# Kernel optimization log

Hardware: AMD Instinct MI355X
Metric: run time of the kernel (lower is better)

Reference implementation:

```python
import jax, jax.numpy as jnp
import numpy as np

N_BOOKS = 8
TAU_Q = 5.0

def setup_inputs() -> dict:
    key = jax.random.key(0)
    k1, k2, k3 = jax.random.split(key, 3)
    N, D_in = 65536, 512
    D = 512          # N_books * L_word
    N_words = 256
    x = jax.random.normal(k1, (N, D_in), dtype=jnp.float32)
    # xavier-uniform-like scale for fc weight [D_out, D_in]
    lim_w = float(np.sqrt(6.0 / (D_in + D)))
    W = jax.random.uniform(k2, (D, D_in), dtype=jnp.float32, minval=-lim_w, maxval=lim_w)
    b = jnp.zeros((D,), dtype=jnp.float32)
    lim_c = float(np.sqrt(6.0 / (N_words + D)))
    C = jax.random.uniform(k3, (N_words, D), dtype=jnp.float32, minval=-lim_c, maxval=lim_c)
    return {"x": x, "W": W, "b": b, "C": C}

def reference(x, W, b, C):
    # fc: X = x @ W^T + b  -> [N, D]
    X = x @ W.T + b
    N, D = X.shape
    M = C.shape[0]
    L = D // N_BOOKS
    Xb = X.reshape(N, N_BOOKS, L)          # [N, B, L]
    Cb = C.reshape(M, N_BOOKS, L)          # [M, B, L]
    x2 = jnp.sum(Xb * Xb, axis=-1)[:, :, None]           # [N, B, 1]
    c2 = jnp.sum(Cb * Cb, axis=-1).T[None, :, :]         # [1, B, M]
    xc = jnp.einsum('nbl,mbl->nbm', Xb, Cb)              # [N, B, M]
    dist = x2 + c2 - 2.0 * xc
    soft = jax.nn.softmax(-TAU_Q * dist, axis=-1)        # softmax over codewords
    # weighted codebook sum per book, then concat books -> [N, D]
    Z = jnp.einsum('nbm,mbl->nbl', soft, Cb).reshape(N, D)
    return X, Z
```

## Files before the change

kernel.cpp:

```cpp
#include <hip/hip_runtime.h>
#include <cstdint>
#include <cstddef>

#define N_ROWS   65536
#define D_IN     512
#define D_OUT    512
#define N_WORDS  256
#define N_BOOKS  8
#define TAU      5.0f
#define LOG2E    1.44269504088896340736f

typedef __attribute__((ext_vector_type(8))) short short8;
typedef __attribute__((ext_vector_type(4))) float f32x4;

__device__ __forceinline__ unsigned short f2bf(float f) {
    __bf16 h = (__bf16)f;
    return __builtin_bit_cast(unsigned short, h);
}
__device__ __forceinline__ float bf2f(unsigned short h) {
    unsigned u = ((unsigned)h) << 16;
    return __builtin_bit_cast(float, u);
}

__global__ __launch_bounds__(256) void prep_codebook(
        const float* __restrict__ C, const float* __restrict__ W,
        unsigned short* __restrict__ packA, unsigned short* __restrict__ packB,
        unsigned short* __restrict__ packW, float* __restrict__ nc2) {
    const int gid = blockIdx.x * 256 + threadIdx.x;
    if (gid < 131072) {
        const int i  = gid & 7;
        const int l  = (gid >> 3) & 63;
        const int mf = (gid >> 9) & 15;
        const int ks = (gid >> 13) & 1;
        const int b  = gid >> 14;
        const int row = (l & 15) + 16 * mf;
        const int col = b * 64 + (l >> 4) * 8 + i + 32 * ks;
        packA[gid] = f2bf(C[(size_t)row * D_IN + col]);
    } else if (gid < 262144) {
        const int g   = gid - 131072;
        const int i   = g & 7;
        const int l   = (g >> 3) & 63;
        const int n2  = (g >> 9) & 3;
        const int ks2 = (g >> 11) & 7;
        const int b   = g >> 14;
        const int m   = 32 * ks2 + 16 * (i >> 2) + 4 * (l >> 4) + (i & 3);
        const int col = b * 64 + n2 * 16 + (l & 15);
        packB[g] = f2bf(C[(size_t)m * D_IN + col]);
    } else if (gid < 524288) {
        const int h  = gid - 262144;
        const int i  = h & 7;
        const int l  = (h >> 3) & 63;
        const int cf = (h >> 9) & 7;
        const int kk = (h >> 12) & 15;
        const int bn = h >> 16;
        packW[h] = f2bf(W[(size_t)(bn * 128 + cf * 16 + (l & 15)) * D_IN
                          + kk * 32 + (l >> 4) * 8 + i]);
    } else if (gid < 526336) {
        const int t = gid - 524288;
        const int b = t >> 8, m = t & 255;
        const float* cp = C + (size_t)m * D_IN + b * 64;
        float s = 0.f;
        for (int l = 0; l < 64; ++l) {
            const float v = bf2f(f2bf(cp[l]));
            s = fmaf(v, v, s);
        }
        nc2[t] = -TAU * LOG2E * s;
    }
}

__global__ __launch_bounds__(512, 1) void fused_fc_quant(
        const float* __restrict__ x, const unsigned short* __restrict__ packW,
        const float* __restrict__ bias,
        const unsigned short* __restrict__ packA,
        const unsigned short* __restrict__ packB,
        const float* __restrict__ nc2g,
        float* __restrict__ X, float* __restrict__ Z) {
    __shared__ unsigned short Asm[2][64 * 40];
    __shared__ __attribute__((aligned(16))) unsigned short Xb[8][32 * 72];
    __shared__ float nc2s[2048];

    const int tid  = threadIdx.x;
    const int n0   = blockIdx.x * 64;
    const int lane = tid & 63;
    const int w    = tid >> 6;
    const int lo = lane & 15, hi = lane >> 4;
    const int bn  = w >> 1;
    const int wc4 = (w & 1) * 4;

    const int row_s = tid >> 3;
    const int fq    = (tid & 7) << 2;

    reinterpret_cast<float4*>(nc2s)[tid] = reinterpret_cast<const float4*>(nc2g)[tid];

    float biasv[4];
    #pragma unroll
    for (int cf = 0; cf < 4; ++cf) biasv[cf] = bias[w * 64 + cf * 16 + lo];

    f32x4 acc[4][4];
    #pragma unroll
    for (int i = 0; i < 4; ++i)
        #pragma unroll
        for (int j = 0; j < 4; ++j) acc[i][j] = (f32x4){0.f, 0.f, 0.f, 0.f};

    float4 rx[2];
    short8 rw[2][4];
    rx[0] = *reinterpret_cast<const float4*>(&x[(size_t)(n0 + row_s) * D_IN + fq]);
    #pragma unroll
    for (int cf = 0; cf < 4; ++cf)
        rw[0][cf] = *reinterpret_cast<const short8*>(
            packW + ((size_t)((bn * 16 + 0) * 8 + wc4 + cf) * 64 + lane) * 8);
    {
        ushort4 p;
        p.x = f2bf(rx[0].x); p.y = f2bf(rx[0].y);
        p.z = f2bf(rx[0].z); p.w = f2bf(rx[0].w);
        *reinterpret_cast<ushort4*>(&Asm[0][row_s * 40 + fq]) = p;
    }
    rx[1] = *reinterpret_cast<const float4*>(&x[(size_t)(n0 + row_s) * D_IN + 32 + fq]);
    #pragma unroll
    for (int cf = 0; cf < 4; ++cf)
        rw[1][cf] = *reinterpret_cast<const short8*>(
            packW + ((size_t)((bn * 16 + 1) * 8 + wc4 + cf) * 64 + lane) * 8);
    __syncthreads();

    #pragma unroll
    for (int kk = 0; kk < 16; ++kk) {
        const int cur = kk & 1;
        short8 aW[4];
        #pragma unroll
        for (int cf = 0; cf < 4; ++cf) aW[cf] = rw[cur][cf];
        if (kk < 14) {
            rx[cur] = *reinterpret_cast<const float4*>(
                &x[(size_t)(n0 + row_s) * D_IN + (kk + 2) * 32 + fq]);
            #pragma unroll
            for (int cf = 0; cf < 4; ++cf)
                rw[cur][cf] = *reinterpret_cast<const short8*>(
                    packW + ((size_t)((bn * 16 + kk + 2) * 8 + wc4 + cf) * 64 + lane) * 8);
        }
        short8 a[4];
        #pragma unroll
        for (int fm = 0; fm < 4; ++fm)
            a[fm] = *reinterpret_cast<const short8*>(&Asm[cur][(fm * 16 + lo) * 40 + hi * 8]);
        #pragma unroll
        for (int fm = 0; fm < 4; ++fm)
            #pragma unroll
            for (int cf = 0; cf < 4; ++cf)
                acc[fm][cf] = __builtin_amdgcn_mfma_f32_16x16x32_bf16(
                    a[fm], aW[cf], acc[fm][cf], 0, 0, 0);
        if (kk < 15) {
            const float4 v = rx[cur ^ 1];
            ushort4 p;
            p.x = f2bf(v.x); p.y = f2bf(v.y); p.z = f2bf(v.z); p.w = f2bf(v.w);
            *reinterpret_cast<ushort4*>(&Asm[cur ^ 1][row_s * 40 + fq]) = p;
            __syncthreads();
        }
    }

    const float S2 = 2.0f * TAU * LOG2E;
    #pragma unroll
    for (int h = 0; h < 2; ++h) {
        #pragma unroll
        for (int fmh = 0; fmh < 2; ++fmh) {
            const int fm = h * 2 + fmh;
            #pragma unroll
            for (int cf = 0; cf < 4; ++cf)
                #pragma unroll
                for (int j = 0; j < 4; ++j) {
                    const float v = acc[fm][cf][j] + biasv[cf];
                    __builtin_nontemporal_store(
                        v, &X[(size_t)(n0 + h * 32 + fmh * 16 + hi * 4 + j) * D_OUT
                              + w * 64 + cf * 16 + lo]);
                    Xb[w][(fmh * 16 + hi * 4 + j) * 72 + cf * 16 + lo] = f2bf(v);
                }
        }
        asm volatile("s_waitcnt lgkmcnt(0)" ::: "memory");

        short8 xf[2][2];
        #pragma unroll
        for (int g = 0; g < 2; ++g)
            #pragma unroll
            for (int ks = 0; ks < 2; ++ks)
                xf[g][ks] = *reinterpret_cast<const short8*>(
                    &Xb[w][(g * 16 + lo) * 72 + ks * 32 + hi * 8]);

        f32x4 qa[2][16];
        #pragma unroll
        for (int g = 0; g < 2; ++g)
            #pragma unroll
            for (int mf = 0; mf < 16; ++mf) qa[g][mf] = (f32x4){0.f, 0.f, 0.f, 0.f};
        #pragma unroll
        for (int ks = 0; ks < 2; ++ks)
            #pragma unroll
            for (int mf = 0; mf < 16; ++mf) {
                const short8 cfr = *reinterpret_cast<const short8*>(
                    packA + ((size_t)((w * 2 + ks) * 16 + mf) * 64 + lane) * 8);
                qa[0][mf] = __builtin_amdgcn_mfma_f32_16x16x32_bf16(cfr, xf[0][ks], qa[0][mf], 0, 0, 0);
                qa[1][mf] = __builtin_amdgcn_mfma_f32_16x16x32_bf16(cfr, xf[1][ks], qa[1][mf], 0, 0, 0);
            }

        float inv[2];
        #pragma unroll
        for (int g = 0; g < 2; ++g) {
            float s = 0.f;
            #pragma unroll
            for (int mf = 0; mf < 16; ++mf) {
                const f32x4 nv = *reinterpret_cast<const f32x4*>(
                    &nc2s[w * 256 + mf * 16 + hi * 4]);
                const float p0 = exp2f(fmaf(qa[g][mf][0], S2, nv[0]));
                const float p1 = exp2f(fmaf(qa[g][mf][1], S2, nv[1]));
                const float p2 = exp2f(fmaf(qa[g][mf][2], S2, nv[2]));
                const float p3 = exp2f(fmaf(qa[g][mf][3], S2, nv[3]));
                qa[g][mf][0] = p0; qa[g][mf][1] = p1;
                qa[g][mf][2] = p2; qa[g][mf][3] = p3;
                s += (p0 + p1) + (p2 + p3);
            }
            s += __shfl_xor(s, 16, 64);
            s += __shfl_xor(s, 32, 64);
            inv[g] = 1.0f / s;
        }

        f32x4 acc2[2][4];
        #pragma unroll
        for (int g = 0; g < 2; ++g)
            #pragma unroll
            for (int n2 = 0; n2 < 4; ++n2) acc2[g][n2] = (f32x4){0.f, 0.f, 0.f, 0.f};
        #pragma unroll
        for (int ks2 = 0; ks2 < 8; ++ks2) {
            short8 pa[2];
            #pragma unroll
            for (int g = 0; g < 2; ++g) {
                pa[g][0] = (short)f2bf(qa[g][2 * ks2][0]);
                pa[g][1] = (short)f2bf(qa[g][2 * ks2][1]);
                pa[g][2] = (short)f2bf(qa[g][2 * ks2][2]);
                pa[g][3] = (short)f2bf(qa[g][2 * ks2][3]);
                pa[g][4] = (short)f2bf(qa[g][2 * ks2 + 1][0]);
                pa[g][5] = (short)f2bf(qa[g][2 * ks2 + 1][1]);
                pa[g][6] = (short)f2bf(qa[g][2 * ks2 + 1][2]);
                pa[g][7] = (short)f2bf(qa[g][2 * ks2 + 1][3]);
            }
            #pragma unroll
            for (int n2 = 0; n2 < 4; ++n2) {
                const short8 bv = *reinterpret_cast<const short8*>(
                    packB + ((size_t)((w * 8 + ks2) * 4 + n2) * 64 + lane) * 8);
                acc2[0][n2] = __builtin_amdgcn_mfma_f32_16x16x32_bf16(pa[0], bv, acc2[0][n2], 0, 0, 0);
                acc2[1][n2] = __builtin_amdgcn_mfma_f32_16x16x32_bf16(pa[1], bv, acc2[1][n2], 0, 0, 0);
            }
        }

        #pragma unroll
        for (int g = 0; g < 2; ++g) {
            float invr[4];
            #pragma unroll
            for (int j = 0; j < 4; ++j) invr[j] = __shfl(inv[g], hi * 4 + j, 64);
            #pragma unroll
            for (int n2 = 0; n2 < 4; ++n2)
                #pragma unroll
                for (int j = 0; j < 4; ++j)
                    __builtin_nontemporal_store(
                        acc2[g][n2][j] * invr[j],
                        &Z[(size_t)(n0 + h * 32 + g * 16 + hi * 4 + j) * D_OUT
                           + w * 64 + n2 * 16 + lo]);
        }
    }
}

extern "C" void kernel_launch(void* const* d_in, const int* in_sizes, int n_in,
                              void* d_out, int out_size, void* d_ws, size_t ws_size,
                              hipStream_t stream) {
    const float* x = (const float*)d_in[0];
    const float* W = (const float*)d_in[1];
    const float* b = (const float*)d_in[2];
    const float* C = (const float*)d_in[3];

    float* X = (float*)d_out;
    float* Z = X + (size_t)N_ROWS * D_OUT;

    unsigned short* packA = (unsigned short*)d_ws;
    unsigned short* packB = packA + 131072;
    unsigned short* packW = packB + 131072;
    float*          nc2g  = (float*)(packW + 262144);

    prep_codebook<<<dim3(2056), dim3(256), 0, stream>>>(C, W, packA, packB, packW, nc2g);
    fused_fc_quant<<<dim3(N_ROWS / 64), dim3(512), 0, stream>>>(
        x, packW, b, packA, packB, nc2g, X, Z);
}
```

Measured before the change: 168.2 us.

## Halve rows per block, stage full x tile in LDS, pack softmax probs early

Each block now handles 32 rows instead of 64. The whole 32x512 x tile is converted to bf16 and staged in LDS up front, which removes the per-k-step double buffering and the barriers inside the FC loop. The quantization stage processes the codeword dimension in two halves and packs the exp values straight into bf16 pairs, so fewer live fp32 registers are needed. The launch bound no longer forces one block per CU, aiming for higher occupancy. The cost is twice as many blocks, so packW, packA and packB are re-read twice as often per row, and the LDS footprint per block grows.

```diff
diff --git a/kernel.cpp b/kernel.cpp
--- a/kernel.cpp
+++ b/kernel.cpp
@@ -12,6 +12,7 @@
 
 typedef __attribute__((ext_vector_type(8))) short short8;
 typedef __attribute__((ext_vector_type(4))) float f32x4;
+typedef __attribute__((ext_vector_type(4))) unsigned uint4v;
 
 __device__ __forceinline__ unsigned short f2bf(float f) {
     __bf16 h = (__bf16)f;
@@ -68,198 +69,190 @@
     }
 }
 
-__global__ __launch_bounds__(512, 1) void fused_fc_quant(
+__global__ __launch_bounds__(512) void fused_fc_quant(
         const float* __restrict__ x, const unsigned short* __restrict__ packW,
         const float* __restrict__ bias,
         const unsigned short* __restrict__ packA,
         const unsigned short* __restrict__ packB,
         const float* __restrict__ nc2g,
         float* __restrict__ X, float* __restrict__ Z) {
-    __shared__ unsigned short Asm[2][64 * 40];
+    __shared__ __attribute__((aligned(16))) unsigned short xAll[32 * 520];
     __shared__ __attribute__((aligned(16))) unsigned short Xb[8][32 * 72];
     __shared__ float nc2s[2048];
 
     const int tid  = threadIdx.x;
-    const int n0   = blockIdx.x * 64;
+    const int n0   = blockIdx.x * 32;
     const int lane = tid & 63;
     const int w    = tid >> 6;
     const int lo = lane & 15, hi = lane >> 4;
     const int bn  = w >> 1;
     const int wc4 = (w & 1) * 4;
 
-    const int row_s = tid >> 3;
-    const int fq    = (tid & 7) << 2;
-
     reinterpret_cast<float4*>(nc2s)[tid] = reinterpret_cast<const float4*>(nc2g)[tid];
 
+    #pragma unroll
+    for (int it = 0; it < 8; ++it) {
+        const int idx = it * 512 + tid;
+        const int row = idx >> 7;
+        const int f4  = idx & 127;
+        const float4 v = *reinterpret_cast<const float4*>(
+            &x[(size_t)(n0 + row) * D_IN + f4 * 4]);
+        ushort4 p;
+        p.x = f2bf(v.x); p.y = f2bf(v.y); p.z = f2bf(v.z); p.w = f2bf(v.w);
+        *reinterpret_cast<ushort4*>(&xAll[row * 520 + f4 * 4]) = p;
+    }
+
     float biasv[4];
     #pragma unroll
     for (int cf = 0; cf < 4; ++cf) biasv[cf] = bias[w * 64 + cf * 16 + lo];
 
-    f32x4 acc[4][4];
-    #pragma unroll
-    for (int i = 0; i < 4; ++i)
-        #pragma unroll
-        for (int j = 0; j < 4; ++j) acc[i][j] = (f32x4){0.f, 0.f, 0.f, 0.f};
-
-    float4 rx[2];
+    __syncthreads();
+
+    f32x4 acc[2][4];
+    #pragma unroll
+    for (int fm = 0; fm < 2; ++fm)
+        #pragma unroll
+        for (int cf = 0; cf < 4; ++cf) acc[fm][cf] = (f32x4){0.f, 0.f, 0.f, 0.f};
+
     short8 rw[2][4];
-    rx[0] = *reinterpret_cast<const float4*>(&x[(size_t)(n0 + row_s) * D_IN + fq]);
-    #pragma unroll
-    for (int cf = 0; cf < 4; ++cf)
+    #pragma unroll
+    for (int cf = 0; cf < 4; ++cf) {
         rw[0][cf] = *reinterpret_cast<const short8*>(
             packW + ((size_t)((bn * 16 + 0) * 8 + wc4 + cf) * 64 + lane) * 8);
-    {
-        ushort4 p;
-        p.x = f2bf(rx[0].x); p.y = f2bf(rx[0].y);
-        p.z = f2bf(rx[0].z); p.w = f2bf(rx[0].w);
-        *reinterpret_cast<ushort4*>(&Asm[0][row_s * 40 + fq]) = p;
-    }
-    rx[1] = *reinterpret_cast<const float4*>(&x[(size_t)(n0 + row_s) * D_IN + 32 + fq]);
-    #pragma unroll
-    for (int cf = 0; cf < 4; ++cf)
         rw[1][cf] = *reinterpret_cast<const short8*>(
             packW + ((size_t)((bn * 16 + 1) * 8 + wc4 + cf) * 64 + lane) * 8);
-    __syncthreads();
-
+    }
     #pragma unroll
     for (int kk = 0; kk < 16; ++kk) {
-        const int cur = kk & 1;
         short8 aW[4];
         #pragma unroll
-        for (int cf = 0; cf < 4; ++cf) aW[cf] = rw[cur][cf];
+        for (int cf = 0; cf < 4; ++cf) aW[cf] = rw[kk & 1][cf];
         if (kk < 14) {
-            rx[cur] = *reinterpret_cast<const float4*>(
-                &x[(size_t)(n0 + row_s) * D_IN + (kk + 2) * 32 + fq]);
             #pragma unroll
             for (int cf = 0; cf < 4; ++cf)
-                rw[cur][cf] = *reinterpret_cast<const short8*>(
+                rw[kk & 1][cf] = *reinterpret_cast<const short8*>(
                     packW + ((size_t)((bn * 16 + kk + 2) * 8 + wc4 + cf) * 64 + lane) * 8);
         }
-        short8 a[4];
-        #pragma unroll
-        for (int fm = 0; fm < 4; ++fm)
-            a[fm] = *reinterpret_cast<const short8*>(&Asm[cur][(fm * 16 + lo) * 40 + hi * 8]);
-        #pragma unroll
-        for (int fm = 0; fm < 4; ++fm)
+        short8 a[2];
+        #pragma unroll
+        for (int fm = 0; fm < 2; ++fm)
+            a[fm] = *reinterpret_cast<const short8*>(
+                &xAll[(fm * 16 + lo) * 520 + kk * 32 + hi * 8]);
+        #pragma unroll
+        for (int fm = 0; fm < 2; ++fm)
             #pragma unroll
             for (int cf = 0; cf < 4; ++cf)
                 acc[fm][cf] = __builtin_amdgcn_mfma_f32_16x16x32_bf16(
                     a[fm], aW[cf], acc[fm][cf], 0, 0, 0);
-        if (kk < 15) {
-            const float4 v = rx[cur ^ 1];
-            ushort4 p;
-            p.x = f2bf(v.x); p.y = f2bf(v.y); p.z = f2bf(v.z); p.w = f2bf(v.w);
-            *reinterpret_cast<ushort4*>(&Asm[cur ^ 1][row_s * 40 + fq]) = p;
-            __syncthreads();
-        }
-    }
+    }
+
+    #pragma unroll
+    for (int fm = 0; fm < 2; ++fm)
+        #pragma unroll
+        for (int cf = 0; cf < 4; ++cf)
+            #pragma unroll
+            for (int j = 0; j < 4; ++j) {
+                const float v = acc[fm][cf][j] + biasv[cf];
+                __builtin_nontemporal_store(
+                    v, &X[(size_t)(n0 + fm * 16 + hi * 4 + j) * D_OUT
+                          + w * 64 + cf * 16 + lo]);
+                Xb[w][(fm * 16 + hi * 4 + j) * 72 + cf * 16 + lo] = f2bf(v);
+            }
+    asm volatile("s_waitcnt lgkmcnt(0)" ::: "memory");
+
+    short8 xf[2][2];
+    #pragma unroll
+    for (int g = 0; g < 2; ++g)
+        #pragma unroll
+        for (int ks = 0; ks < 2; ++ks)
+            xf[g][ks] = *reinterpret_cast<const short8*>(
+                &Xb[w][(g * 16 + lo) * 72 + ks * 32 + hi * 8]);
 
     const float S2 = 2.0f * TAU * LOG2E;
-    #pragma unroll
-    for (int h = 0; h < 2; ++h) {
-        #pragma unroll
-        for (int fmh = 0; fmh < 2; ++fmh) {
-            const int fm = h * 2 + fmh;
-            #pragma unroll
-            for (int cf = 0; cf < 4; ++cf)
-                #pragma unroll
-                for (int j = 0; j < 4; ++j) {
-                    const float v = acc[fm][cf][j] + biasv[cf];
-                    __builtin_nontemporal_store(
-                        v, &X[(size_t)(n0 + h * 32 + fmh * 16 + hi * 4 + j) * D_OUT
-                              + w * 64 + cf * 16 + lo]);
-                    Xb[w][(fmh * 16 + hi * 4 + j) * 72 + cf * 16 + lo] = f2bf(v);
-                }
-        }
-        asm volatile("s_waitcnt lgkmcnt(0)" ::: "memory");
-
-        short8 xf[2][2];
+    float ssum[2] = {0.f, 0.f};
+    unsigned pk[2][2][16];
+
+    #pragma unroll
+    for (int H = 0; H < 2; ++H) {
+        f32x4 qa[2][8];
         #pragma unroll
         for (int g = 0; g < 2; ++g)
             #pragma unroll
-            for (int ks = 0; ks < 2; ++ks)
-                xf[g][ks] = *reinterpret_cast<const short8*>(
-                    &Xb[w][(g * 16 + lo) * 72 + ks * 32 + hi * 8]);
-
-        f32x4 qa[2][16];
-        #pragma unroll
-        for (int g = 0; g < 2; ++g)
-            #pragma unroll
-            for (int mf = 0; mf < 16; ++mf) qa[g][mf] = (f32x4){0.f, 0.f, 0.f, 0.f};
+            for (int mf = 0; mf < 8; ++mf) qa[g][mf] = (f32x4){0.f, 0.f, 0.f, 0.f};
         #pragma unroll
         for (int ks = 0; ks < 2; ++ks)
             #pragma unroll
-            for (int mf = 0; mf < 16; ++mf) {
+            for (int mf = 0; mf < 8; ++mf) {
                 const short8 cfr = *reinterpret_cast<const short8*>(
-                    packA + ((size_t)((w * 2 + ks) * 16 + mf) * 64 + lane) * 8);
-                qa[0][mf] = __builtin_amdgcn_mfma_f32_16x16x32_bf16(cfr, xf[0][ks], qa[0][mf], 0, 0, 0);
-                qa[1][mf] = __builtin_amdgcn_mfma_f32_16x16x32_bf16(cfr, xf[1][ks], qa[1][mf], 0, 0, 0);
+                    packA + ((size_t)((w * 2 + ks) * 16 + H * 8 + mf) * 64 + lane) * 8);
+                qa[0][mf] = __builtin_amdgcn_mfma_f32_16x16x32_bf16(
+                    cfr, xf[0][ks], qa[0][mf], 0, 0, 0);
+                qa[1][mf] = __builtin_amdgcn_mfma_f32_16x16x32_bf16(
+                    cfr, xf[1][ks], qa[1][mf], 0, 0, 0);
             }
-
-        float inv[2];
-        #pragma unroll
-        for (int g = 0; g < 2; ++g) {
-            float s = 0.f;
-            #pragma unroll
-            for (int mf = 0; mf < 16; ++mf) {
-                const f32x4 nv = *reinterpret_cast<const f32x4*>(
-                    &nc2s[w * 256 + mf * 16 + hi * 4]);
+        #pragma unroll
+        for (int mf = 0; mf < 8; ++mf) {
+            const f32x4 nv = *reinterpret_cast<const f32x4*>(
+                &nc2s[w * 256 + (H * 8 + mf) * 16 + hi * 4]);
+            #pragma unroll
+            for (int g = 0; g < 2; ++g) {
                 const float p0 = exp2f(fmaf(qa[g][mf][0], S2, nv[0]));
                 const float p1 = exp2f(fmaf(qa[g][mf][1], S2, nv[1]));
                 const float p2 = exp2f(fmaf(qa[g][mf][2], S2, nv[2]));
                 const float p3 = exp2f(fmaf(qa[g][mf][3], S2, nv[3]));
-                qa[g][mf][0] = p0; qa[g][mf][1] = p1;
-                qa[g][mf][2] = p2; qa[g][mf][3] = p3;
-                s += (p0 + p1) + (p2 + p3);
+                ssum[g] += (p0 + p1) + (p2 + p3);
+                pk[g][H][mf * 2]     = ((unsigned)f2bf(p1) << 16) | f2bf(p0);
+                pk[g][H][mf * 2 + 1] = ((unsigned)f2bf(p3) << 16) | f2bf(p2);
             }
-            s += __shfl_xor(s, 16, 64);
-            s += __shfl_xor(s, 32, 64);
-            inv[g] = 1.0f / s;
-        }
-
-        f32x4 acc2[2][4];
-        #pragma unroll
-        for (int g = 0; g < 2; ++g)
-            #pragma unroll
-            for (int n2 = 0; n2 < 4; ++n2) acc2[g][n2] = (f32x4){0.f, 0.f, 0.f, 0.f};
-        #pragma unroll
-        for (int ks2 = 0; ks2 < 8; ++ks2) {
-            short8 pa[2];
-            #pragma unroll
-            for (int g = 0; g < 2; ++g) {
-                pa[g][0] = (short)f2bf(qa[g][2 * ks2][0]);
-                pa[g][1] = (short)f2bf(qa[g][2 * ks2][1]);
-                pa[g][2] = (short)f2bf(qa[g][2 * ks2][2]);
-                pa[g][3] = (short)f2bf(qa[g][2 * ks2][3]);
-                pa[g][4] = (short)f2bf(qa[g][2 * ks2 + 1][0]);
-                pa[g][5] = (short)f2bf(qa[g][2 * ks2 + 1][1]);
-                pa[g][6] = (short)f2bf(qa[g][2 * ks2 + 1][2]);
-                pa[g][7] = (short)f2bf(qa[g][2 * ks2 + 1][3]);
-            }
-            #pragma unroll
-            for (int n2 = 0; n2 < 4; ++n2) {
-                const short8 bv = *reinterpret_cast<const short8*>(
-                    packB + ((size_t)((w * 8 + ks2) * 4 + n2) * 64 + lane) * 8);
-                acc2[0][n2] = __builtin_amdgcn_mfma_f32_16x16x32_bf16(pa[0], bv, acc2[0][n2], 0, 0, 0);
-                acc2[1][n2] = __builtin_amdgcn_mfma_f32_16x16x32_bf16(pa[1], bv, acc2[1][n2], 0, 0, 0);
-            }
-        }
-
-        #pragma unroll
-        for (int g = 0; g < 2; ++g) {
-            float invr[4];
-            #pragma unroll
-            for (int j = 0; j < 4; ++j) invr[j] = __shfl(inv[g], hi * 4 + j, 64);
-            #pragma unroll
-            for (int n2 = 0; n2 < 4; ++n2)
-                #pragma unroll
-                for (int j = 0; j < 4; ++j)
-                    __builtin_nontemporal_store(
-                        acc2[g][n2][j] * invr[j],
-                        &Z[(size_t)(n0 + h * 32 + g * 16 + hi * 4 + j) * D_OUT
-                           + w * 64 + n2 * 16 + lo]);
-        }
+        }
+    }
+
+    float inv[2];
+    #pragma unroll
+    for (int g = 0; g < 2; ++g) {
+        float s = ssum[g];
+        s += __shfl_xor(s, 16, 64);
+        s += __shfl_xor(s, 32, 64);
+        inv[g] = 1.0f / s;
+    }
+
+    f32x4 acc2[2][4];
+    #pragma unroll
+    for (int g = 0; g < 2; ++g)
+        #pragma unroll
+        for (int n2 = 0; n2 < 4; ++n2) acc2[g][n2] = (f32x4){0.f, 0.f, 0.f, 0.f};
+    #pragma unroll
+    for (int ks2 = 0; ks2 < 8; ++ks2) {
+        const int H  = ks2 >> 2;
+        const int sp = ks2 & 3;
+        const uint4v ua0 = {pk[0][H][4 * sp], pk[0][H][4 * sp + 1],
+                            pk[0][H][4 * sp + 2], pk[0][H][4 * sp + 3]};
+        const uint4v ua1 = {pk[1][H][4 * sp], pk[1][H][4 * sp + 1],
+                            pk[1][H][4 * sp + 2], pk[1][H][4 * sp + 3]};
+        const short8 pa0 = __builtin_bit_cast(short8, ua0);
+        const short8 pa1 = __builtin_bit_cast(short8, ua1);
+        #pragma unroll
+        for (int n2 = 0; n2 < 4; ++n2) {
+            const short8 bv = *reinterpret_cast<const short8*>(
+                packB + ((size_t)((w * 8 + ks2) * 4 + n2) * 64 + lane) * 8);
+            acc2[0][n2] = __builtin_amdgcn_mfma_f32_16x16x32_bf16(pa0, bv, acc2[0][n2], 0, 0, 0);
+            acc2[1][n2] = __builtin_amdgcn_mfma_f32_16x16x32_bf16(pa1, bv, acc2[1][n2], 0, 0, 0);
+        }
+    }
+
+    #pragma unroll
+    for (int g = 0; g < 2; ++g) {
+        float invr[4];
+        #pragma unroll
+        for (int j = 0; j < 4; ++j) invr[j] = __shfl(inv[g], hi * 4 + j, 64);
+        #pragma unroll
+        for (int n2 = 0; n2 < 4; ++n2)
+            #pragma unroll
+            for (int j = 0; j < 4; ++j)
+                __builtin_nontemporal_store(
+                    acc2[g][n2][j] * invr[j],
+                    &Z[(size_t)(n0 + g * 16 + hi * 4 + j) * D_OUT
+                       + w * 64 + n2 * 16 + lo]);
     }
 }
 
@@ -280,6 +273,6 @@
     float*          nc2g  = (float*)(packW + 262144);
 
     prep_codebook<<<dim3(2056), dim3(256), 0, stream>>>(C, W, packA, packB, packW, nc2g);
-    fused_fc_quant<<<dim3(N_ROWS / 64), dim3(512), 0, stream>>>(
+    fused_fc_quant<<<dim3(N_ROWS / 32), dim3(512), 0, stream>>>(
         x, packW, b, packA, packB, nc2g, X, Z);
 }
```

New measurement: 216.0 us. 28.4% more time.
